# Kernel optimization log

Measured on AMD Instinct MI355X. Metric: run time of the kernel, lower is better.

Reference implementation:

```python
import jax, jax.numpy as jnp
import numpy as np

B, NQ, S, H, NH = 2, 1024, 4096, 1024, 16
HD = H // NH
EPS = 1e-6


def layer_norm(x, gamma, beta):
    mu = jnp.mean(x, axis=-1, keepdims=True)
    var = jnp.mean(jnp.square(x - mu), axis=-1, keepdims=True)
    return (x - mu) * jax.lax.rsqrt(var + EPS) * gamma + beta


def setup_inputs() -> dict:
    key = jax.random.key(0)
    ks = jax.random.split(key, 6)
    queries = jax.random.normal(ks[0], (B, NQ, H), dtype=jnp.float32)
    keys_values = jax.random.normal(ks[1], (B, S, H), dtype=jnp.float32)
    attention_mask = jax.random.uniform(ks[2], (B, S)) > 0.1
    attention_mask = attention_mask.at[:, 0].set(True)
    # params (torch Linear stored transposed here so y = x @ W + b)
    W_qkv = jax.random.normal(ks[3], (H, 3 * H), dtype=jnp.float32) * 0.02
    b_qkv = jnp.zeros((3 * H,), dtype=jnp.float32)
    W_out = jax.random.normal(ks[4], (H, H), dtype=jnp.float32) * 0.02
    b_out = jnp.zeros((H,), dtype=jnp.float32)
    gamma = jnp.ones((H,), dtype=jnp.float32)
    beta = jnp.zeros((H,), dtype=jnp.float32)
    return {"queries": queries, "keys_values": keys_values,
            "attention_mask": attention_mask,
            "W_qkv": W_qkv, "b_qkv": b_qkv, "W_out": W_out, "b_out": b_out,
            "gamma": gamma, "beta": beta}


def reference(queries, keys_values, attention_mask, W_qkv, b_qkv, W_out, b_out, gamma, beta):
    # shared LayerNorm + shared qkv projection applied to both streams
    q_in = layer_norm(queries, gamma, beta)
    kv_in = layer_norm(keys_values, gamma, beta)
    q = (q_in @ W_qkv + b_qkv)[..., :H]                    # [B,NQ,H]
    kv = kv_in @ W_qkv + b_qkv
    k = kv[..., H:2 * H]                                    # [B,S,H]
    v = kv[..., 2 * H:]                                     # [B,S,H]
    q = q.reshape(B, NQ, NH, HD)
    k = k.reshape(B, S, NH, HD)
    v = v.reshape(B, S, NH, HD)
    scale = 1.0 / np.sqrt(HD).astype(np.float32)
    scores = jnp.einsum('bqhd,bkhd->bhqk', q, k) * scale    # [B,NH,NQ,S]
    neg_inf = jnp.finfo(scores.dtype).min
    scores = jnp.where(attention_mask[:, None, None, :], scores, neg_inf)
    attn = jax.nn.softmax(scores, axis=-1)
    out = jnp.einsum('bhqk,bkhd->bqhd', attn, v).reshape(B, NQ, H)
    return out @ W_out + b_out
```

## Files before the change

kernel.cpp:

```cpp
#include <hip/hip_runtime.h>
#include <stdint.h>

#define DEVI __device__ __forceinline__

constexpr int Bb = 2, NQ = 1024, S = 4096, H = 1024, NH = 16, HD = 64;
constexpr int NSPLIT = 4, SLEN = S / NSPLIT;

typedef __bf16 bf16x8 __attribute__((ext_vector_type(8)));
typedef float f32x4 __attribute__((ext_vector_type(4)));
typedef int i32x4 __attribute__((ext_vector_type(4)));
typedef unsigned short u16;
typedef u16 u16x8 __attribute__((ext_vector_type(8)));

DEVI u16 f2bf(float f) {
  union { float f; unsigned u; } v; v.f = f;
  unsigned r = (v.u + 0x7fffu + ((v.u >> 16) & 1u)) >> 16;
  return (u16)r;
}

DEVI float bf2f(u16 x) {
  union { unsigned u; float f; } v; v.u = ((unsigned)x) << 16;
  return v.f;
}

DEVI float fexp2(float x) {
#if __has_builtin(__builtin_amdgcn_exp2f)
  return __builtin_amdgcn_exp2f(x);
#else
  return exp2f(x);
#endif
}

DEVI void gload_lds16(const void* g, void* lds) {
  __builtin_amdgcn_global_load_lds(
      (const __attribute__((address_space(1))) void*)(uintptr_t)g,
      (__attribute__((address_space(3))) void*)(uint32_t)(uintptr_t)lds,
      16, 0, 0);
}

DEVI void ln_body(const float* __restrict__ x, const float* __restrict__ gamma,
                  const float* __restrict__ beta, u16* __restrict__ out, int row) {
  int lane = threadIdx.x & 63;
  const float4* xr = (const float4*)(x + (size_t)row * H);
  float4 v[4];
  float s = 0.f, s2 = 0.f;
#pragma unroll
  for (int i = 0; i < 4; ++i) {
    v[i] = xr[lane + i * 64];
    s += v[i].x + v[i].y + v[i].z + v[i].w;
    s2 += v[i].x * v[i].x + v[i].y * v[i].y + v[i].z * v[i].z + v[i].w * v[i].w;
  }
#pragma unroll
  for (int d = 1; d < 64; d <<= 1) { s += __shfl_xor(s, d); s2 += __shfl_xor(s2, d); }
  float mu = s * (1.f / H);
  float rstd = rsqrtf(s2 * (1.f / H) - mu * mu + 1e-6f);
  u16* orow = out + (size_t)row * H;
  const float4* g4 = (const float4*)gamma;
  const float4* b4 = (const float4*)beta;
#pragma unroll
  for (int i = 0; i < 4; ++i) {
    float4 g = g4[lane + i * 64], bb = b4[lane + i * 64];
    ushort4 o;
    o.x = f2bf((v[i].x - mu) * rstd * g.x + bb.x);
    o.y = f2bf((v[i].y - mu) * rstd * g.y + bb.y);
    o.z = f2bf((v[i].z - mu) * rstd * g.z + bb.z);
    o.w = f2bf((v[i].w - mu) * rstd * g.w + bb.w);
    *(ushort4*)(orow + (size_t)(lane + i * 64) * 4) = o;
  }
}

__global__ __launch_bounds__(256) void prep_kernel(
    const unsigned char* __restrict__ mraw, unsigned char* __restrict__ maskN,
    const float* __restrict__ queries, const float* __restrict__ keys_values,
    const float* __restrict__ gamma, const float* __restrict__ beta,
    u16* __restrict__ Xq, u16* __restrict__ Xkv,
    const float* __restrict__ W_qkv, const float* __restrict__ W_out,
    u16* __restrict__ Wtq, u16* __restrict__ Wto) {
  __shared__ int isByte;
  __shared__ float tile[32][33];
  const int b = blockIdx.x;
  if (b == 0) {
    if (threadIdx.x == 0) isByte = 0;
    __syncthreads();
    int any = 0;
    for (int p = threadIdx.x; p < Bb * S; p += 256)
      if ((p & 3) && mraw[p]) any = 1;
    if (any) atomicOr(&isByte, 1);
    __syncthreads();
    const int bytemode = isByte;
    for (int i = threadIdx.x; i < Bb * S; i += 256) {
      unsigned char v = bytemode ? (unsigned char)(mraw[i] != 0)
                                 : (unsigned char)(((const int*)mraw)[i] != 0);
      maskN[i] = v;
    }
  } else if (b < 513) {
    ln_body(queries, gamma, beta, Xq, (b - 1) * 4 + (threadIdx.x >> 6));
  } else if (b < 2561) {
    ln_body(keys_values, gamma, beta, Xkv, (b - 513) * 4 + (threadIdx.x >> 6));
  } else {
    const float* in; u16* out; int C, t;
    if (b < 5633) { t = b - 2561; in = W_qkv; out = Wtq; C = 3 * H; }
    else          { t = b - 5633; in = W_out; out = Wto; C = H; }
    const int nbx = C / 32;
    int c0 = (t % nbx) * 32, r0 = (t / nbx) * 32;
    int tx = threadIdx.x & 31, ty = threadIdx.x >> 5;
#pragma unroll
    for (int i = 0; i < 32; i += 8)
      tile[ty + i][tx] = in[(size_t)(r0 + ty + i) * C + c0 + tx];
    __syncthreads();
#pragma unroll
    for (int i = 0; i < 32; i += 8)
      out[(size_t)(c0 + ty + i) * H + r0 + tx] = f2bf(tile[tx][ty + i]);
  }
}

#define GEMM_CORE(Ag, Bg)                                                        \
  f32x4 acc[4][4] = {};                                                          \
  {                                                                              \
    for (int k0 = 0; k0 < 1024; k0 += 32) {                                      \
      gload_lds16(Ag + (size_t)(c0 >> 2) * 1024 + k0 + (c0 & 3) * 8, Ash + c0 * 8); \
      gload_lds16(Ag + (size_t)(c1 >> 2) * 1024 + k0 + (c1 & 3) * 8, Ash + c1 * 8); \
      gload_lds16(Bg + (size_t)(c0 >> 2) * 1024 + k0 + (c0 & 3) * 8, Bsh + c0 * 8); \
      gload_lds16(Bg + (size_t)(c1 >> 2) * 1024 + k0 + (c1 & 3) * 8, Bsh + c1 * 8); \
      asm volatile("s_waitcnt vmcnt(0)" ::: "memory");                           \
      __syncthreads();                                                           \
      bf16x8 af[4], bfr[4];                                                      \
      _Pragma("unroll") for (int m = 0; m < 4; ++m)                              \
          af[m] = *(const bf16x8*)(Ash + (wr + m * 16 + fr) * 32 + fq * 8);      \
      _Pragma("unroll") for (int n = 0; n < 4; ++n)                              \
          bfr[n] = *(const bf16x8*)(Bsh + (wc + n * 16 + fr) * 32 + fq * 8);     \
      _Pragma("unroll") for (int m = 0; m < 4; ++m)                              \
          _Pragma("unroll") for (int n = 0; n < 4; ++n)                          \
              acc[m][n] = __builtin_amdgcn_mfma_f32_16x16x32_bf16(af[m], bfr[n], acc[m][n], 0, 0, 0); \
      __syncthreads();                                                           \
    }                                                                            \
  }

__global__ __launch_bounds__(256) void gemm_q_kernel(
    const u16* __restrict__ Xq, const u16* __restrict__ Wtq,
    const float* __restrict__ bias, u16* __restrict__ Qbuf) {
  __shared__ __align__(16) u16 Ash[128 * 32];
  __shared__ __align__(16) u16 Bsh[128 * 32];
  const int tid = threadIdx.x, w = tid >> 6, lane = tid & 63;
  const int c0 = tid, c1 = tid + 256;
  const int wr = (w >> 1) * 64, wc = (w & 1) * 64;
  const int fr = lane & 15, fq = lane >> 4;
  const int brow = blockIdx.y * 128, bcol = blockIdx.x * 128;
  const u16* Ag = Xq + (size_t)brow * 1024;
  const u16* Bg = Wtq + (size_t)bcol * 1024;
  GEMM_CORE(Ag, Bg)
  constexpr float QSCALE = 0.125f * 1.4426950408889634f;
#pragma unroll
  for (int m = 0; m < 4; ++m)
#pragma unroll
    for (int n = 0; n < 4; ++n) {
      const int c = bcol + wc + n * 16 + fr;
      const int r0 = brow + wr + m * 16 + fq * 4;
#pragma unroll
      for (int i = 0; i < 4; ++i) {
        int r = r0 + i;
        Qbuf[((((size_t)(r >> 10)) * NH + (c >> 6)) * NQ + (r & (NQ - 1))) * HD + (c & 63)] =
            f2bf((acc[m][n][i] + bias[c]) * QSCALE);
      }
    }
}

__global__ __launch_bounds__(512, 2) void gemm_kv_kernel(
    const u16* __restrict__ Xkv, const u16* __restrict__ WtqKV,
    const float* __restrict__ bias, u16* __restrict__ KVbuf) {
  __shared__ __align__(16) u16 Abuf[4][256 * 32];
  __shared__ __align__(16) u16 Bbuf[4][256 * 32];
  const int tid = threadIdx.x, wid = tid >> 6, lane = tid & 63;
  const int fr = lane & 15, fq = lane >> 4;
  const int wr = (wid >> 2) * 128, wc = (wid & 3) * 64;
  const int bid = blockIdx.x;
  const int xcd = bid & 7, loc = bid >> 3;
  const int by = xcd * 4 + (loc & 3), bx = loc >> 2;
  const u16* Ag = Xkv + (size_t)(by * 256) * 1024;
  const u16* Bg = WtqKV + (size_t)(bx * 256) * 1024;

  f32x4 acc[8][4] = {};

  auto stage = [&](int tt) {
    const int k0 = tt * 32;
    u16* Ad = &Abuf[tt & 3][0];
    u16* Bd = &Bbuf[tt & 3][0];
#pragma unroll
    for (int l = 0; l < 2; ++l) {
      int ci = tid + l * 512;
      int row = ci >> 2, ch = ci & 3;
      int chs = ch ^ ((row >> 1) & 3);
      gload_lds16(Ag + (size_t)row * 1024 + k0 + chs * 8, Ad + ci * 8);
      gload_lds16(Bg + (size_t)row * 1024 + k0 + chs * 8, Bd + ci * 8);
    }
  };

#define KV_ITER(T, VM)                                                          \
  {                                                                             \
    asm volatile("s_waitcnt vmcnt(" #VM ")" ::: "memory");                      \
    __syncthreads();                                                            \
    const u16* Ac = &Abuf[(T) & 3][0];                                          \
    const u16* Bc = &Bbuf[(T) & 3][0];                                          \
    bf16x8 af[8], bfv[4];                                                       \
    _Pragma("unroll") for (int m = 0; m < 8; ++m) {                             \
      int row = wr + m * 16 + fr;                                               \
      af[m] = *(const bf16x8*)(Ac + row * 32 + (fq ^ ((row >> 1) & 3)) * 8);    \
    }                                                                           \
    _Pragma("unroll") for (int n = 0; n < 4; ++n) {                             \
      int row = wc + n * 16 + fr;                                               \
      bfv[n] = *(const bf16x8*)(Bc + row * 32 + (fq ^ ((row >> 1) & 3)) * 8);   \
    }                                                                           \
    if ((T) + 3 < 32) stage((T) + 3);                                           \
    __builtin_amdgcn_s_setprio(1);                                              \
    _Pragma("unroll") for (int m = 0; m < 8; ++m)                               \
      _Pragma("unroll") for (int n = 0; n < 4; ++n)                             \
        acc[m][n] = __builtin_amdgcn_mfma_f32_16x16x32_bf16(af[m], bfv[n], acc[m][n], 0, 0, 0); \
    __builtin_amdgcn_s_setprio(0);                                              \
  }

  stage(0);
  stage(1);
  stage(2);
  for (int t = 0; t < 29; ++t) KV_ITER(t, 8)
  KV_ITER(29, 8)
  KV_ITER(30, 4)
  KV_ITER(31, 0)
#undef KV_ITER

#pragma unroll
  for (int m = 0; m < 8; ++m)
#pragma unroll
    for (int n = 0; n < 4; ++n) {
      const int c = bx * 256 + wc + n * 16 + fr;
      const int r0 = by * 256 + wr + m * 16 + fq * 4;
      const float bv = bias[c];
      if (c >= 1024) {
        int bb = r0 >> 12, kv = r0 & (S - 1);
        int cc = c - 1024, head = cc >> 6, d = cc & 63;
        ushort4 o;
        o.x = f2bf(acc[m][n][0] + bv);
        o.y = f2bf(acc[m][n][1] + bv);
        o.z = f2bf(acc[m][n][2] + bv);
        o.w = f2bf(acc[m][n][3] + bv);
        u16* vb = KVbuf + (size_t)Bb * NH * S * HD;
        *(ushort4*)(vb + (((size_t)(bb * NH + head)) * HD + d) * S + kv) = o;
      } else {
#pragma unroll
        for (int i = 0; i < 4; ++i) {
          int r = r0 + i;
          KVbuf[((((size_t)(r >> 12)) * NH + (c >> 6)) * S + (r & (S - 1))) * HD + (c & 63)] =
              f2bf(acc[m][n][i] + bv);
        }
      }
    }
}

__global__ __launch_bounds__(256) void gemm_out_kernel(
    const u16* __restrict__ A, const u16* __restrict__ Bt,
    const float* __restrict__ bias, float* __restrict__ outp) {
  __shared__ __align__(16) u16 Ash[128 * 32];
  __shared__ __align__(16) u16 Bsh[128 * 32];
  const int tid = threadIdx.x, w = tid >> 6, lane = tid & 63;
  const int c0 = tid, c1 = tid + 256;
  const int wr = (w >> 1) * 64, wc = (w & 1) * 64;
  const int fr = lane & 15, fq = lane >> 4;
  const int brow = blockIdx.y * 128, bcol = blockIdx.x * 128;
  const u16* Ag = A + (size_t)brow * 1024;
  const u16* Bg = Bt + (size_t)bcol * 1024;
  GEMM_CORE(Ag, Bg)
#pragma unroll
  for (int m = 0; m < 4; ++m)
#pragma unroll
    for (int n = 0; n < 4; ++n) {
      const int c = bcol + wc + n * 16 + fr;
      const int r0 = brow + wr + m * 16 + fq * 4;
#pragma unroll
      for (int i = 0; i < 4; ++i)
        outp[(size_t)(r0 + i) * H + c] = acc[m][n][i] + bias[c];
    }
}

__global__ __launch_bounds__(512, 4) void attn_kernel(
    const u16* __restrict__ Qb, const u16* __restrict__ Kb,
    const u16* __restrict__ Vt, const unsigned char* __restrict__ mask,
    u16* __restrict__ Opart, float2* __restrict__ ml) {
  __shared__ __align__(16) char smem[34816];
  u16* Ktile = (u16*)smem;
  u16* Vtile = Ktile + 8192;
  float* Mb = (float*)(Vtile + 8192);
  const int bflat = blockIdx.x;
  const int r = bflat & 7, idx = bflat >> 3;
  const int q0 = (idx & 3) * 256;
  const int g = (idx >> 2) * 8 + r;
  const int bh = g & 31, z = g >> 5;
  const int b = bh >> 4, kv0 = z * SLEN;
  const int tid = threadIdx.x, w = tid >> 6, lane = tid & 63;
  const int fr = lane & 15, fq = lane >> 4, fr7 = fr & 7;
  const u16* QgA = Qb + ((size_t)bh * NQ + q0 + w * 32) * HD;
  const u16* QgB = QgA + 16 * HD;
  const u16* Kg = Kb + (size_t)bh * S * HD;
  const u16* Vg = Vt + (size_t)bh * HD * S;
  const unsigned char* mg = mask + (size_t)b * S + kv0;

  const int rs = tid >> 3, gs = (tid & 7) ^ (rs & 7);

  bf16x8 qfA0 = *(const bf16x8*)(QgA + fr * HD + fq * 8);
  bf16x8 qfA1 = *(const bf16x8*)(QgA + fr * HD + 32 + fq * 8);
  bf16x8 qfB0 = *(const bf16x8*)(QgB + fr * HD + fq * 8);
  bf16x8 qfB1 = *(const bf16x8*)(QgB + fr * HD + 32 + fq * 8);

  const int A0 = ((((fq << 1)) & 3) * 16 + fr) << 2;
  const int A1 = ((((fq << 1) + 1) & 3) * 16 + fr) << 2;
  const bool lofq = (fq < 2);

  f32x4 oaccA[4] = {}, oaccB[4] = {};
  float mrowA = -1e30f, lrowA = 0.f, mrowB = -1e30f, lrowB = 0.f;

  if (tid < 64) Mb[tid] = mg[tid] ? 0.f : -1e30f;
  gload_lds16(Kg + (size_t)(kv0 + rs) * HD + gs * 8, Ktile + tid * 8);
  gload_lds16(Vg + (size_t)rs * S + kv0 + gs * 8, Vtile + tid * 8);
  asm volatile("s_waitcnt vmcnt(0)" ::: "memory");
  __syncthreads();

  int cur = 0;
  for (int kt = 0; kt < SLEN; kt += 64) {
    const int nb = cur ^ 1, kn = kt + 64;
    if (kn < SLEN) {
      if (tid < 64) Mb[nb * 64 + tid] = mg[kn + tid] ? 0.f : -1e30f;
      gload_lds16(Kg + (size_t)(kv0 + kn + rs) * HD + gs * 8, Ktile + nb * 4096 + tid * 8);
      gload_lds16(Vg + (size_t)rs * S + kv0 + kn + gs * 8, Vtile + nb * 4096 + tid * 8);
    }

    const u16* Kc = Ktile + cur * 4096;
    const u16* Vc = Vtile + cur * 4096;

    float svA[4][4], svB[4][4];
    __builtin_amdgcn_s_setprio(1);
#pragma unroll
    for (int nt = 0; nt < 4; ++nt) {
      const u16* kb2 = Kc + (nt * 16 + fr) * 64;
      bf16x8 k0v = *(const bf16x8*)(kb2 + ((fq) ^ fr7) * 8);
      bf16x8 k1v = *(const bf16x8*)(kb2 + ((4 + fq) ^ fr7) * 8);
      f32x4 tA = {}, tB = {};
      tA = __builtin_amdgcn_mfma_f32_16x16x32_bf16(k0v, qfA0, tA, 0, 0, 0);
      tA = __builtin_amdgcn_mfma_f32_16x16x32_bf16(k1v, qfA1, tA, 0, 0, 0);
      tB = __builtin_amdgcn_mfma_f32_16x16x32_bf16(k0v, qfB0, tB, 0, 0, 0);
      tB = __builtin_amdgcn_mfma_f32_16x16x32_bf16(k1v, qfB1, tB, 0, 0, 0);
      float4 mb = *(const float4*)&Mb[cur * 64 + nt * 16 + fq * 4];
      svA[nt][0] = tA[0] + mb.x; svA[nt][1] = tA[1] + mb.y;
      svA[nt][2] = tA[2] + mb.z; svA[nt][3] = tA[3] + mb.w;
      svB[nt][0] = tB[0] + mb.x; svB[nt][1] = tB[1] + mb.y;
      svB[nt][2] = tB[2] + mb.z; svB[nt][3] = tB[3] + mb.w;
    }
    __builtin_amdgcn_s_setprio(0);

    float pmaxA, pmaxB;
    {
      float a0 = fmaxf(fmaxf(svA[0][0], svA[0][1]), fmaxf(svA[0][2], svA[0][3]));
      float a1 = fmaxf(fmaxf(svA[1][0], svA[1][1]), fmaxf(svA[1][2], svA[1][3]));
      float a2 = fmaxf(fmaxf(svA[2][0], svA[2][1]), fmaxf(svA[2][2], svA[2][3]));
      float a3 = fmaxf(fmaxf(svA[3][0], svA[3][1]), fmaxf(svA[3][2], svA[3][3]));
      pmaxA = fmaxf(fmaxf(a0, a1), fmaxf(a2, a3));
      float b0 = fmaxf(fmaxf(svB[0][0], svB[0][1]), fmaxf(svB[0][2], svB[0][3]));
      float b1 = fmaxf(fmaxf(svB[1][0], svB[1][1]), fmaxf(svB[1][2], svB[1][3]));
      float b2 = fmaxf(fmaxf(svB[2][0], svB[2][1]), fmaxf(svB[2][2], svB[2][3]));
      float b3 = fmaxf(fmaxf(svB[3][0], svB[3][1]), fmaxf(svB[3][2], svB[3][3]));
      pmaxB = fmaxf(fmaxf(b0, b1), fmaxf(b2, b3));
    }
    if (__any(pmaxA > mrowA + 12.f)) {
      pmaxA = fmaxf(pmaxA, __shfl_xor(pmaxA, 16));
      pmaxA = fmaxf(pmaxA, __shfl_xor(pmaxA, 32));
      float nm = fmaxf(mrowA, pmaxA);
      float al = fexp2(mrowA - nm);
      mrowA = nm; lrowA *= al;
#pragma unroll
      for (int nt = 0; nt < 4; ++nt)
#pragma unroll
        for (int i = 0; i < 4; ++i) oaccA[nt][i] *= al;
    }
    if (__any(pmaxB > mrowB + 12.f)) {
      pmaxB = fmaxf(pmaxB, __shfl_xor(pmaxB, 16));
      pmaxB = fmaxf(pmaxB, __shfl_xor(pmaxB, 32));
      float nm = fmaxf(mrowB, pmaxB);
      float al = fexp2(mrowB - nm);
      mrowB = nm; lrowB *= al;
#pragma unroll
      for (int nt = 0; nt < 4; ++nt)
#pragma unroll
        for (int i = 0; i < 4; ++i) oaccB[nt][i] *= al;
    }

    float pA[4][4], pB[4][4];
#pragma unroll
    for (int nt = 0; nt < 4; ++nt)
#pragma unroll
      for (int i = 0; i < 4; ++i) {
        pA[nt][i] = fexp2(svA[nt][i] - mrowA);
        pB[nt][i] = fexp2(svB[nt][i] - mrowB);
      }
    {
      float s0 = (pA[0][0] + pA[0][1]) + (pA[0][2] + pA[0][3]);
      float s1 = (pA[1][0] + pA[1][1]) + (pA[1][2] + pA[1][3]);
      float s2 = (pA[2][0] + pA[2][1]) + (pA[2][2] + pA[2][3]);
      float s3 = (pA[3][0] + pA[3][1]) + (pA[3][2] + pA[3][3]);
      lrowA += (s0 + s1) + (s2 + s3);
      float t0 = (pB[0][0] + pB[0][1]) + (pB[0][2] + pB[0][3]);
      float t1 = (pB[1][0] + pB[1][1]) + (pB[1][2] + pB[1][3]);
      float t2 = (pB[2][0] + pB[2][1]) + (pB[2][2] + pB[2][3]);
      float t3 = (pB[3][0] + pB[3][1]) + (pB[3][2] + pB[3][3]);
      lrowB += (t0 + t1) + (t2 + t3);
    }

    int pkA[4][2], pkB[4][2];
#pragma unroll
    for (int nt = 0; nt < 4; ++nt) {
      asm("v_cvt_pk_bf16_f32 %0, %1, %2" : "=v"(pkA[nt][0]) : "v"(pA[nt][0]), "v"(pA[nt][1]));
      asm("v_cvt_pk_bf16_f32 %0, %1, %2" : "=v"(pkA[nt][1]) : "v"(pA[nt][2]), "v"(pA[nt][3]));
      asm("v_cvt_pk_bf16_f32 %0, %1, %2" : "=v"(pkB[nt][0]) : "v"(pB[nt][0]), "v"(pB[nt][1]));
      asm("v_cvt_pk_bf16_f32 %0, %1, %2" : "=v"(pkB[nt][1]) : "v"(pB[nt][2]), "v"(pB[nt][3]));
    }

#pragma unroll
    for (int b2 = 0; b2 < 2; ++b2) {
      i32x4 wvA, wvB;
      {
        int w0a = __builtin_amdgcn_ds_bpermute(A0, pkA[2 * b2][0]);
        int w0b = __builtin_amdgcn_ds_bpermute(A0, pkA[2 * b2 + 1][0]);
        int w1a = __builtin_amdgcn_ds_bpermute(A0, pkA[2 * b2][1]);
        int w1b = __builtin_amdgcn_ds_bpermute(A0, pkA[2 * b2 + 1][1]);
        int w2a = __builtin_amdgcn_ds_bpermute(A1, pkA[2 * b2][0]);
        int w2b = __builtin_amdgcn_ds_bpermute(A1, pkA[2 * b2 + 1][0]);
        int w3a = __builtin_amdgcn_ds_bpermute(A1, pkA[2 * b2][1]);
        int w3b = __builtin_amdgcn_ds_bpermute(A1, pkA[2 * b2 + 1][1]);
        wvA[0] = lofq ? w0a : w0b;
        wvA[1] = lofq ? w1a : w1b;
        wvA[2] = lofq ? w2a : w2b;
        wvA[3] = lofq ? w3a : w3b;
      }
      {
        int w0a = __builtin_amdgcn_ds_bpermute(A0, pkB[2 * b2][0]);
        int w0b = __builtin_amdgcn_ds_bpermute(A0, pkB[2 * b2 + 1][0]);
        int w1a = __builtin_amdgcn_ds_bpermute(A0, pkB[2 * b2][1]);
        int w1b = __builtin_amdgcn_ds_bpermute(A0, pkB[2 * b2 + 1][1]);
        int w2a = __builtin_amdgcn_ds_bpermute(A1, pkB[2 * b2][0]);
        int w2b = __builtin_amdgcn_ds_bpermute(A1, pkB[2 * b2 + 1][0]);
        int w3a = __builtin_amdgcn_ds_bpermute(A1, pkB[2 * b2][1]);
        int w3b = __builtin_amdgcn_ds_bpermute(A1, pkB[2 * b2 + 1][1]);
        wvB[0] = lofq ? w0a : w0b;
        wvB[1] = lofq ? w1a : w1b;
        wvB[2] = lofq ? w2a : w2b;
        wvB[3] = lofq ? w3a : w3b;
      }
      bf16x8 pfragA = __builtin_bit_cast(bf16x8, wvA);
      bf16x8 pfragB = __builtin_bit_cast(bf16x8, wvB);
      __builtin_amdgcn_s_setprio(1);
#pragma unroll
      for (int nt = 0; nt < 4; ++nt) {
        const u16* vb2 = Vc + (nt * 16 + fr) * 64;
        bf16x8 vf = *(const bf16x8*)(vb2 + ((b2 * 4 + fq) ^ fr7) * 8);
        oaccA[nt] = __builtin_amdgcn_mfma_f32_16x16x32_bf16(vf, pfragA, oaccA[nt], 0, 0, 0);
        oaccB[nt] = __builtin_amdgcn_mfma_f32_16x16x32_bf16(vf, pfragB, oaccB[nt], 0, 0, 0);
      }
      __builtin_amdgcn_s_setprio(0);
    }

    asm volatile("s_waitcnt vmcnt(0)" ::: "memory");
    __syncthreads();
    cur = nb;
  }

  lrowA += __shfl_xor(lrowA, 16);
  lrowA += __shfl_xor(lrowA, 32);
  lrowB += __shfl_xor(lrowB, 16);
  lrowB += __shfl_xor(lrowB, 32);
  if (fq == 0) {
    ml[((size_t)z * 32 + bh) * NQ + q0 + w * 32 + fr] = float2{mrowA, lrowA};
    ml[((size_t)z * 32 + bh) * NQ + q0 + w * 32 + 16 + fr] = float2{mrowB, lrowB};
  }

  float* tb = (float*)smem + w * 1088;
  const int qloc = lane >> 2, dl = lane & 3;
#pragma unroll
  for (int gsel = 0; gsel < 2; ++gsel) {
    const f32x4* oc = gsel ? oaccB : oaccA;
#pragma unroll
    for (int nt = 0; nt < 4; ++nt)
#pragma unroll
      for (int i = 0; i < 4; ++i)
        tb[fr * 68 + nt * 16 + fq * 4 + i] = oc[nt][i];
    const float* trow = tb + qloc * 68 + dl * 16;
    u16* gdst = Opart +
        (((size_t)z * 32 + bh) * NQ + q0 + w * 32 + gsel * 16 + qloc) * 64 + dl * 16;
    u16x8 o0, o1;
#pragma unroll
    for (int j = 0; j < 8; ++j) {
      o0[j] = f2bf(trow[j]);
      o1[j] = f2bf(trow[8 + j]);
    }
    *(u16x8*)gdst = o0;
    *(u16x8*)(gdst + 8) = o1;
  }
}

__global__ __launch_bounds__(256) void combine_kernel(
    const u16* __restrict__ Opart, const float2* __restrict__ ml,
    u16* __restrict__ out) {
  const int bh = blockIdx.y, b = bh >> 4, h = bh & 15;
  const int q = blockIdx.x * 64 + (threadIdx.x >> 2);
  const int dl = threadIdx.x & 3;
  float2 mm[NSPLIT];
  float M = -1e30f;
#pragma unroll
  for (int zz = 0; zz < NSPLIT; ++zz) {
    mm[zz] = ml[((size_t)zz * 32 + bh) * NQ + q];
    M = fmaxf(M, mm[zz].x);
  }
  float wz[NSPLIT], lsum = 0.f;
#pragma unroll
  for (int zz = 0; zz < NSPLIT; ++zz) {
    wz[zz] = fexp2(mm[zz].x - M);
    lsum += mm[zz].y * wz[zz];
  }
  const float inv = 1.f / lsum;
  float acc[16] = {};
#pragma unroll
  for (int zz = 0; zz < NSPLIT; ++zz) {
    const u16* op = Opart + (((size_t)zz * 32 + bh) * NQ + q) * 64 + dl * 16;
    u16x8 a0 = *(const u16x8*)op;
    u16x8 a1 = *(const u16x8*)(op + 8);
    float wi = wz[zz] * inv;
#pragma unroll
    for (int j = 0; j < 8; ++j) {
      acc[j] += wi * bf2f(a0[j]);
      acc[8 + j] += wi * bf2f(a1[j]);
    }
  }
  u16* orow = out + ((size_t)b * NQ + q) * H + h * HD + dl * 16;
  u16x8 o0, o1;
#pragma unroll
  for (int j = 0; j < 8; ++j) {
    o0[j] = f2bf(acc[j]);
    o1[j] = f2bf(acc[8 + j]);
  }
  *(u16x8*)orow = o0;
  *(u16x8*)(orow + 8) = o1;
}

extern "C" void kernel_launch(void* const* d_in, const int* in_sizes, int n_in,
                              void* d_out, int out_size, void* d_ws, size_t ws_size,
                              hipStream_t stream) {
  const float* queries = (const float*)d_in[0];
  const float* keys_values = (const float*)d_in[1];
  const void* amask = d_in[2];
  const float* W_qkv = (const float*)d_in[3];
  const float* b_qkv = (const float*)d_in[4];
  const float* W_out = (const float*)d_in[5];
  const float* b_out = (const float*)d_in[6];
  const float* gamma = (const float*)d_in[7];
  const float* beta = (const float*)d_in[8];

  char* ws = (char*)d_ws;
  unsigned char* maskN = (unsigned char*)ws;
  u16* Xq = (u16*)(ws + 8192);
  u16* Xkv = Xq + (size_t)Bb * NQ * H;
  u16* Wtq = Xkv + (size_t)Bb * S * H;
  u16* Wto = Wtq + (size_t)3 * H * H;
  u16* Qbuf = Wto + (size_t)H * H;
  u16* Kbuf = Qbuf + (size_t)Bb * NQ * H;
  u16* Aout = Kbuf + (size_t)2 * Bb * S * H;
  u16* Opart = (u16*)(ws + 8192);
  float2* ml = (float2*)((char*)Opart + (size_t)NSPLIT * 32 * NQ * 64 * 2);

  hipLaunchKernelGGL(prep_kernel, dim3(6657), dim3(256), 0, stream,
                     (const unsigned char*)amask, maskN, queries, keys_values,
                     gamma, beta, Xq, Xkv, W_qkv, W_out, Wtq, Wto);
  hipLaunchKernelGGL(gemm_q_kernel, dim3(8, 16), dim3(256), 0, stream,
                     Xq, Wtq, b_qkv, Qbuf);
  hipLaunchKernelGGL(gemm_kv_kernel, dim3(256), dim3(512), 0, stream,
                     Xkv, Wtq + (size_t)H * H, b_qkv + H, Kbuf);
  hipLaunchKernelGGL(attn_kernel, dim3(NQ / 256 * Bb * NH * NSPLIT), dim3(512), 0, stream,
                     Qbuf, Kbuf, Kbuf + (size_t)Bb * S * H, maskN, Opart, ml);
  hipLaunchKernelGGL(combine_kernel, dim3(NQ / 64, Bb * NH), dim3(256), 0, stream,
                     Opart, ml, Aout);
  hipLaunchKernelGGL(gemm_out_kernel, dim3(H / 128, Bb * NQ / 128), dim3(256), 0, stream,
                     Aout, Wto, b_out, (float*)d_out);
}
```

Before: 173.0 us.

## Merge Q and KV projection GEMMs into one launch; double attention KV tile size

The separate Q projection GEMM is folded into the KV projection kernel: 32 extra 256x256 blocks compute the Q projection with the same pipelined core, which removes one launch and lets the Q work fill the tail of the KV GEMM. The attention kernel now stages 128-key tiles (K and V with new swizzles) per barrier and processes them as two 64-key halves, halving the number of sync and wait points. This raises attention LDS use from about 34KB to about 66KB per block, which may cut occupancy below the declared four blocks per CU.

```diff
diff --git a/kernel.cpp b/kernel.cpp
--- a/kernel.cpp
+++ b/kernel.cpp
@@ -136,48 +136,31 @@
     }                                                                            \
   }
 
-__global__ __launch_bounds__(256) void gemm_q_kernel(
-    const u16* __restrict__ Xq, const u16* __restrict__ Wtq,
-    const float* __restrict__ bias, u16* __restrict__ Qbuf) {
-  __shared__ __align__(16) u16 Ash[128 * 32];
-  __shared__ __align__(16) u16 Bsh[128 * 32];
-  const int tid = threadIdx.x, w = tid >> 6, lane = tid & 63;
-  const int c0 = tid, c1 = tid + 256;
-  const int wr = (w >> 1) * 64, wc = (w & 1) * 64;
-  const int fr = lane & 15, fq = lane >> 4;
-  const int brow = blockIdx.y * 128, bcol = blockIdx.x * 128;
-  const u16* Ag = Xq + (size_t)brow * 1024;
-  const u16* Bg = Wtq + (size_t)bcol * 1024;
-  GEMM_CORE(Ag, Bg)
-  constexpr float QSCALE = 0.125f * 1.4426950408889634f;
-#pragma unroll
-  for (int m = 0; m < 4; ++m)
-#pragma unroll
-    for (int n = 0; n < 4; ++n) {
-      const int c = bcol + wc + n * 16 + fr;
-      const int r0 = brow + wr + m * 16 + fq * 4;
-#pragma unroll
-      for (int i = 0; i < 4; ++i) {
-        int r = r0 + i;
-        Qbuf[((((size_t)(r >> 10)) * NH + (c >> 6)) * NQ + (r & (NQ - 1))) * HD + (c & 63)] =
-            f2bf((acc[m][n][i] + bias[c]) * QSCALE);
-      }
-    }
-}
-
-__global__ __launch_bounds__(512, 2) void gemm_kv_kernel(
-    const u16* __restrict__ Xkv, const u16* __restrict__ WtqKV,
-    const float* __restrict__ bias, u16* __restrict__ KVbuf) {
+__global__ __launch_bounds__(512, 2) void gemm_kvq_kernel(
+    const u16* __restrict__ Xkv, const u16* __restrict__ Xq,
+    const u16* __restrict__ Wtq, const float* __restrict__ b_qkv,
+    u16* __restrict__ KVbuf, u16* __restrict__ Qbuf) {
   __shared__ __align__(16) u16 Abuf[4][256 * 32];
   __shared__ __align__(16) u16 Bbuf[4][256 * 32];
   const int tid = threadIdx.x, wid = tid >> 6, lane = tid & 63;
   const int fr = lane & 15, fq = lane >> 4;
   const int wr = (wid >> 2) * 128, wc = (wid & 3) * 64;
   const int bid = blockIdx.x;
-  const int xcd = bid & 7, loc = bid >> 3;
-  const int by = xcd * 4 + (loc & 3), bx = loc >> 2;
-  const u16* Ag = Xkv + (size_t)(by * 256) * 1024;
-  const u16* Bg = WtqKV + (size_t)(bx * 256) * 1024;
+  const bool isQ = bid >= 256;
+  int by, bx;
+  const u16 *Ap, *Bp;
+  const float* bias;
+  if (!isQ) {
+    const int xcd = bid & 7, loc = bid >> 3;
+    by = xcd * 4 + (loc & 3); bx = loc >> 2;
+    Ap = Xkv; Bp = Wtq + (size_t)H * H; bias = b_qkv + H;
+  } else {
+    const int t = bid - 256;
+    by = t >> 2; bx = t & 3;
+    Ap = Xq; Bp = Wtq; bias = b_qkv;
+  }
+  const u16* Ag = Ap + (size_t)(by * 256) * 1024;
+  const u16* Bg = Bp + (size_t)(bx * 256) * 1024;
 
   f32x4 acc[8][4] = {};
 
@@ -227,6 +210,7 @@
   KV_ITER(31, 0)
 #undef KV_ITER
 
+  constexpr float QSCALE = 0.125f * 1.4426950408889634f;
 #pragma unroll
   for (int m = 0; m < 8; ++m)
 #pragma unroll
@@ -234,7 +218,14 @@
       const int c = bx * 256 + wc + n * 16 + fr;
       const int r0 = by * 256 + wr + m * 16 + fq * 4;
       const float bv = bias[c];
-      if (c >= 1024) {
+      if (isQ) {
+#pragma unroll
+        for (int i = 0; i < 4; ++i) {
+          int r = r0 + i;
+          Qbuf[((((size_t)(r >> 10)) * NH + (c >> 6)) * NQ + (r & (NQ - 1))) * HD + (c & 63)] =
+              f2bf((acc[m][n][i] + bv) * QSCALE);
+        }
+      } else if (c >= 1024) {
         int bb = r0 >> 12, kv = r0 & (S - 1);
         int cc = c - 1024, head = cc >> 6, d = cc & 63;
         ushort4 o;
@@ -284,10 +275,10 @@
     const u16* __restrict__ Qb, const u16* __restrict__ Kb,
     const u16* __restrict__ Vt, const unsigned char* __restrict__ mask,
     u16* __restrict__ Opart, float2* __restrict__ ml) {
-  __shared__ __align__(16) char smem[34816];
+  __shared__ __align__(16) char smem[66560];
   u16* Ktile = (u16*)smem;
-  u16* Vtile = Ktile + 8192;
-  float* Mb = (float*)(Vtile + 8192);
+  u16* Vtile = (u16*)(smem + 32768);
+  float* Mb = (float*)(smem + 65536);
   const int bflat = blockIdx.x;
   const int r = bflat & 7, idx = bflat >> 3;
   const int q0 = (idx & 3) * 256;
@@ -302,7 +293,10 @@
   const u16* Vg = Vt + (size_t)bh * HD * S;
   const unsigned char* mg = mask + (size_t)b * S + kv0;
 
-  const int rs = tid >> 3, gs = (tid & 7) ^ (rs & 7);
+  const int kr0 = tid >> 3, kc0 = (tid & 7) ^ (kr0 & 7);
+  const int kr1 = (tid + 512) >> 3, kc1 = ((tid + 512) & 7) ^ (kr1 & 7);
+  const int vr0 = tid >> 4, vc0 = (tid & 15) ^ (vr0 & 15);
+  const int vr1 = (tid + 512) >> 4, vc1 = ((tid + 512) & 15) ^ (vr1 & 15);
 
   bf16x8 qfA0 = *(const bf16x8*)(QgA + fr * HD + fq * 8);
   bf16x8 qfA1 = *(const bf16x8*)(QgA + fr * HD + 32 + fq * 8);
@@ -316,23 +310,17 @@
   f32x4 oaccA[4] = {}, oaccB[4] = {};
   float mrowA = -1e30f, lrowA = 0.f, mrowB = -1e30f, lrowB = 0.f;
 
-  if (tid < 64) Mb[tid] = mg[tid] ? 0.f : -1e30f;
-  gload_lds16(Kg + (size_t)(kv0 + rs) * HD + gs * 8, Ktile + tid * 8);
-  gload_lds16(Vg + (size_t)rs * S + kv0 + gs * 8, Vtile + tid * 8);
-  asm volatile("s_waitcnt vmcnt(0)" ::: "memory");
-  __syncthreads();
-
-  int cur = 0;
-  for (int kt = 0; kt < SLEN; kt += 64) {
-    const int nb = cur ^ 1, kn = kt + 64;
-    if (kn < SLEN) {
-      if (tid < 64) Mb[nb * 64 + tid] = mg[kn + tid] ? 0.f : -1e30f;
-      gload_lds16(Kg + (size_t)(kv0 + kn + rs) * HD + gs * 8, Ktile + nb * 4096 + tid * 8);
-      gload_lds16(Vg + (size_t)rs * S + kv0 + kn + gs * 8, Vtile + nb * 4096 + tid * 8);
-    }
-
-    const u16* Kc = Ktile + cur * 4096;
-    const u16* Vc = Vtile + cur * 4096;
+  auto stageKV = [&](int buf, int kts) {
+    gload_lds16(Kg + (size_t)(kv0 + kts + kr0) * HD + kc0 * 8, Ktile + buf * 8192 + tid * 8);
+    gload_lds16(Kg + (size_t)(kv0 + kts + kr1) * HD + kc1 * 8, Ktile + buf * 8192 + (tid + 512) * 8);
+    gload_lds16(Vg + (size_t)vr0 * S + kv0 + kts + vc0 * 8, Vtile + buf * 8192 + tid * 8);
+    gload_lds16(Vg + (size_t)vr1 * S + kv0 + kts + vc1 * 8, Vtile + buf * 8192 + (tid + 512) * 8);
+  };
+
+  auto process = [&](int cur, int h) {
+    const u16* Kc = Ktile + cur * 8192 + h * 4096;
+    const u16* Vc = Vtile + cur * 8192;
+    const float* Mc = Mb + cur * 128 + h * 64;
 
     float svA[4][4], svB[4][4];
     __builtin_amdgcn_s_setprio(1);
@@ -346,7 +334,7 @@
       tA = __builtin_amdgcn_mfma_f32_16x16x32_bf16(k1v, qfA1, tA, 0, 0, 0);
       tB = __builtin_amdgcn_mfma_f32_16x16x32_bf16(k0v, qfB0, tB, 0, 0, 0);
       tB = __builtin_amdgcn_mfma_f32_16x16x32_bf16(k1v, qfB1, tB, 0, 0, 0);
-      float4 mb = *(const float4*)&Mb[cur * 64 + nt * 16 + fq * 4];
+      float4 mb = *(const float4*)&Mc[nt * 16 + fq * 4];
       svA[nt][0] = tA[0] + mb.x; svA[nt][1] = tA[1] + mb.y;
       svA[nt][2] = tA[2] + mb.z; svA[nt][3] = tA[3] + mb.w;
       svB[nt][0] = tB[0] + mb.x; svB[nt][1] = tB[1] + mb.y;
@@ -456,14 +444,29 @@
       __builtin_amdgcn_s_setprio(1);
 #pragma unroll
       for (int nt = 0; nt < 4; ++nt) {
-        const u16* vb2 = Vc + (nt * 16 + fr) * 64;
-        bf16x8 vf = *(const bf16x8*)(vb2 + ((b2 * 4 + fq) ^ fr7) * 8);
+        const u16* vb2 = Vc + (nt * 16 + fr) * 128;
+        bf16x8 vf = *(const bf16x8*)(vb2 + ((h * 8 + b2 * 4 + fq) ^ fr) * 8);
         oaccA[nt] = __builtin_amdgcn_mfma_f32_16x16x32_bf16(vf, pfragA, oaccA[nt], 0, 0, 0);
         oaccB[nt] = __builtin_amdgcn_mfma_f32_16x16x32_bf16(vf, pfragB, oaccB[nt], 0, 0, 0);
       }
       __builtin_amdgcn_s_setprio(0);
     }
-
+  };
+
+  if (tid < 128) Mb[tid] = mg[tid] ? 0.f : -1e30f;
+  stageKV(0, 0);
+  asm volatile("s_waitcnt vmcnt(0)" ::: "memory");
+  __syncthreads();
+
+  int cur = 0;
+  for (int kt = 0; kt < SLEN; kt += 128) {
+    const int nb = cur ^ 1, kn = kt + 128;
+    if (kn < SLEN) {
+      if (tid < 128) Mb[nb * 128 + tid] = mg[kn + tid] ? 0.f : -1e30f;
+      stageKV(nb, kn);
+    }
+    process(cur, 0);
+    process(cur, 1);
     asm volatile("s_waitcnt vmcnt(0)" ::: "memory");
     __syncthreads();
     cur = nb;
@@ -574,10 +577,8 @@
   hipLaunchKernelGGL(prep_kernel, dim3(6657), dim3(256), 0, stream,
                      (const unsigned char*)amask, maskN, queries, keys_values,
                      gamma, beta, Xq, Xkv, W_qkv, W_out, Wtq, Wto);
-  hipLaunchKernelGGL(gemm_q_kernel, dim3(8, 16), dim3(256), 0, stream,
-                     Xq, Wtq, b_qkv, Qbuf);
-  hipLaunchKernelGGL(gemm_kv_kernel, dim3(256), dim3(512), 0, stream,
-                     Xkv, Wtq + (size_t)H * H, b_qkv + H, Kbuf);
+  hipLaunchKernelGGL(gemm_kvq_kernel, dim3(288), dim3(512), 0, stream,
+                     Xkv, Xq, Wtq, b_qkv, Kbuf, Qbuf);
   hipLaunchKernelGGL(attn_kernel, dim3(NQ / 256 * Bb * NH * NSPLIT), dim3(512), 0, stream,
                      Qbuf, Kbuf, Kbuf + (size_t)Bb * S * H, maskN, Opart, ml);
   hipLaunchKernelGGL(combine_kernel, dim3(NQ / 64, Bb * NH), dim3(256), 0, stream,
```

Result: slower. 185.1 us (+7.0%).
